# Kernel tuning notes

Hardware: AMD Instinct MI355X
Metric: run time of the kernel (lower is better)

Reference implementation:

```python
import jax, jax.numpy as jnp
import numpy as np

WIDTH = 16
HID = 512
NHEADS = 8
DK = HID // NHEADS
NLAYERS = 2
NHIGHWAY = 2
B = 4
S = 1024
PAD = S + 2 * WIDTH  # padded sequence length


def setup_inputs() -> dict:
    key = jax.random.key(0)
    ks = jax.random.split(key, 10)
    sc = 0.02
    f32 = jnp.float32
    return {
        "inputs": jax.random.normal(ks[0], (B, S, HID), f32),
        "masks": jnp.ones((B, S), jnp.int32),
        # 4 linears (q,k,v,out) per attention, torch Linear layout [out,in]
        "fw_lin_w": sc * jax.random.normal(ks[1], (NLAYERS, 4, HID, HID), f32),
        "fw_lin_b": jnp.zeros((NLAYERS, 4, HID), f32),
        "bw_lin_w": sc * jax.random.normal(ks[2], (NLAYERS, 4, HID, HID), f32),
        "bw_lin_b": jnp.zeros((NLAYERS, 4, HID), f32),
        # Highway: Linear(H, 2H); [:H]=nonlinear part, [H:]=gate (gate bias init 1)
        "fw_hw_w": sc * jax.random.normal(ks[3], (NLAYERS, NHIGHWAY, 2 * HID, HID), f32),
        "fw_hw_b": jnp.zeros((NLAYERS, NHIGHWAY, 2 * HID), f32).at[:, :, HID:].set(1.0),
        "bw_hw_w": sc * jax.random.normal(ks[4], (NLAYERS, NHIGHWAY, 2 * HID, HID), f32),
        "bw_hw_b": jnp.zeros((NLAYERS, NHIGHWAY, 2 * HID), f32).at[:, :, HID:].set(1.0),
        # learned boundary paddings, [width, hidden] per layer
        "fw_pad": sc * jax.random.normal(ks[5], (NLAYERS, WIDTH, HID), f32),
        "bw_pad": sc * jax.random.normal(ks[6], (NLAYERS, WIDTH, HID), f32),
        # relative-position weight vectors, [width+1] per layer
        "fw_rel": sc * jax.random.normal(ks[7], (NLAYERS, WIDTH + 1), f32),
        "bw_rel": sc * jax.random.normal(ks[8], (NLAYERS, WIDTH + 1), f32),
    }


def _band_masks():
    i = jnp.arange(PAD)[:, None]
    j = jnp.arange(PAD)[None, :]
    mf = (j <= i) & (j >= i - WIDTH - 1)          # causal band, width+2 wide
    mb = (j >= i) & (j <= i + WIDTH + 1)          # flipped (anticausal) band
    return mf, mb


def _mha(x, w, b, mask):
    # x: [B, PAD, HID]; w: [4, HID, HID]; b: [4, HID]
    def heads(t):
        return t.reshape(B, PAD, NHEADS, DK).transpose(0, 2, 1, 3)  # bhpd
    q = heads(x @ w[0].T + b[0])
    k = heads(x @ w[1].T + b[1])
    v = heads(x @ w[2].T + b[2])
    scores = jnp.einsum('bhqd,bhkd->bhqk', q, k) / np.sqrt(DK).astype(np.float32)
    scores = jnp.where(mask[None, None], scores, jnp.float32(-1e9))
    p = jax.nn.softmax(scores, axis=-1)
    o = jnp.einsum('bhqk,bhkd->bhqd', p, v)
    o = o.transpose(0, 2, 1, 3).reshape(B, PAD, HID)
    return o @ w[3].T + b[3]


def _highway(x, w, b):
    for i in range(NHIGHWAY):
        proj = x @ w[i].T + b[i]
        nonlin = jax.nn.relu(proj[..., :HID])
        gate = jax.nn.sigmoid(proj[..., HID:])
        x = gate * x + (1.0 - gate) * nonlin
    return x


def _rel(x, w, offset):
    # sum_k w[k] * x[:, offset+k : offset+k+S, :]  (width+1=17 fixed taps)
    out = w[0] * jax.lax.dynamic_slice_in_dim(x, offset, S, 1)
    for k in range(1, WIDTH + 1):
        out = out + w[k] * jax.lax.dynamic_slice_in_dim(x, offset + k, S, 1)
    return out


def _forward(inputs, fw_lin_w, fw_lin_b, bw_lin_w, bw_lin_b,
             fw_hw_w, fw_hw_b, bw_hw_w, bw_hw_b,
             fw_pad, bw_pad, fw_rel, bw_rel):
    mf, mb = _band_masks()
    f = inputs
    bk = inputs
    outs = []
    for l in range(NLAYERS):
        fp = jnp.broadcast_to(fw_pad[l][None], (B, WIDTH, HID))
        bp = jnp.broadcast_to(bw_pad[l][None], (B, WIDTH, HID))
        f_padded = jnp.concatenate([fp, f, bp], axis=1)    # [B, PAD, HID]
        b_padded = jnp.concatenate([fp, bk, bp], axis=1)
        fa = _mha(f_padded, fw_lin_w[l], fw_lin_b[l], mf)
        ba = _mha(b_padded, bw_lin_w[l], bw_lin_b[l], mb)
        # per-step: out[t] = attn[t+width] + rel-position windowed combination
        fo = fa[:, WIDTH:WIDTH + S, :] + _rel(fa, fw_rel[l], 0)
        bo = ba[:, WIDTH:WIDTH + S, :] + _rel(ba, bw_rel[l], WIDTH)
        f = _highway(fo, fw_hw_w[l], fw_hw_b[l])
        bk = _highway(bo, bw_hw_w[l], bw_hw_b[l])
        outs.append(jnp.concatenate([f, bk], axis=-1))
    return jnp.stack(outs, axis=0)  # [NLAYERS, B, S, 2*HID]


def reference(inputs, masks, fw_lin_w, fw_lin_b, bw_lin_w, bw_lin_b,
              fw_hw_w, fw_hw_b, bw_hw_w, bw_hw_b,
              fw_pad, bw_pad, fw_rel, bw_rel):
    # masks is accepted (as in the torch signature) but unused in the body
    return _forward(inputs, fw_lin_w, fw_lin_b, bw_lin_w, bw_lin_b,
                    fw_hw_w, fw_hw_b, bw_hw_w, bw_hw_b,
                    fw_pad, bw_pad, fw_rel, bw_rel)
```

## Files before the change

### kernel.cpp

```cpp
#include <hip/hip_runtime.h>

using s8 = __attribute__((ext_vector_type(8))) short;
using f4 = __attribute__((ext_vector_type(4))) float;

constexpr int WIDTH   = 16;
constexpr int HID     = 512;
constexpr int NHEADS  = 8;
constexpr int DK      = 64;
constexpr int NLAYERS = 2;
constexpr int NHW     = 2;
constexpr int B       = 4;
constexpr int S       = 1024;
constexpr int PAD     = S + 2 * WIDTH;
constexpr int RS      = 1024;
constexpr int K2      = 1024;

__device__ inline size_t caddr(int row, int col) {
    return ((size_t)((row >> 4) * 32 + (col >> 5)) << 9)
         + ((row & 15) << 3) + (((col >> 3) & 3) << 7) + (col & 7);
}

__device__ inline unsigned short f2bf(float x) {
    union { float f; unsigned u; } c; c.f = x;
    unsigned r = c.u + 0x7fffu + ((c.u >> 16) & 1u);
    return (unsigned short)(r >> 16);
}
__device__ inline float bf2f(unsigned short h) {
    union { float f; unsigned u; } c; c.u = ((unsigned)h) << 16; return c.f;
}
__device__ inline void split2(float x, unsigned short& h, unsigned short& l) {
    h = f2bf(x);
    l = f2bf(x - bf2f(h));
}
__device__ inline void store_split8(unsigned short* base, int row, int col,
                                    float4 v0, float4 v1) {
    float v[8] = {v0.x, v0.y, v0.z, v0.w, v1.x, v1.y, v1.z, v1.w};
    unsigned h[4], l[4];
    #pragma unroll
    for (int j = 0; j < 4; ++j) {
        unsigned short h0, l0, h1, l1;
        split2(v[2 * j], h0, l0); split2(v[2 * j + 1], h1, l1);
        h[j] = h0 | ((unsigned)h1 << 16);
        l[j] = l0 | ((unsigned)l1 << 16);
    }
    *(uint4*)(base + caddr(row, col))       = make_uint4(h[0], h[1], h[2], h[3]);
    *(uint4*)(base + caddr(row, col + 512)) = make_uint4(l[0], l[1], l[2], l[3]);
}
__device__ inline void store_split4_c(unsigned short* base, int row, int col,
                                      float4 v) {
    unsigned short h[4], l[4];
    split2(v.x, h[0], l[0]); split2(v.y, h[1], l[1]);
    split2(v.z, h[2], l[2]); split2(v.w, h[3], l[3]);
    uint2 hp, lp;
    hp.x = h[0] | ((unsigned)h[1] << 16); hp.y = h[2] | ((unsigned)h[3] << 16);
    lp.x = l[0] | ((unsigned)l[1] << 16); lp.y = l[2] | ((unsigned)l[3] << 16);
    *(uint2*)(base + caddr(row, col))       = hp;
    *(uint2*)(base + caddr(row, col + 512)) = lp;
}

__device__ inline void xcd_swizzle(int& bx, int& by) {
    const int gx = gridDim.x, gy = gridDim.y;
    const int nwg = gx * gy;
    const int orig = by * gx + bx;
    const int q = nwg >> 3, r = nwg & 7;
    const int x8 = orig & 7, i8 = orig >> 3;
    const int wg = (x8 < r ? x8 * (q + 1) : r * (q + 1) + (x8 - r) * q) + i8;
    bx = wg % gx;
    by = wg / gx;
}

__global__ __launch_bounds__(256) void build_pad_split(
    const float* __restrict__ src0, const float* __restrict__ src1,
    const float* __restrict__ front, const float* __restrict__ back,
    unsigned short* __restrict__ d0, unsigned short* __restrict__ d1)
{
    const float* x = blockIdx.z ? src1 : src0;
    unsigned short* xp2 = blockIdx.z ? d1 : d0;
    int idx = blockIdx.x * 256 + threadIdx.x;
    int c8 = idx & 63;
    int rest = idx >> 6;
    int p = rest % PAD;
    int b = rest / PAD;
    const float* s;
    if (p < WIDTH) {
        s = front + (size_t)p * HID;
    } else if (p < WIDTH + S) {
        s = x + ((size_t)b * S + (p - WIDTH)) * HID;
    } else {
        s = back + (size_t)(p - WIDTH - S) * HID;
    }
    float4 v0 = *(const float4*)(s + c8 * 8);
    float4 v1 = *(const float4*)(s + c8 * 8 + 4);
    store_split8(xp2, b * PAD + p, c8 * 8, v0, v1);
}

__global__ __launch_bounds__(256) void conv_w(
    const float* __restrict__ s0, const float* __restrict__ s1,
    unsigned short* __restrict__ w0, unsigned short* __restrict__ w1)
{
    const float* src = blockIdx.z ? s1 : s0;
    unsigned short* dst = blockIdx.z ? w1 : w0;
    int idx = blockIdx.x * 256 + threadIdx.x;
    int c8 = idx & 63;
    int r  = idx >> 6;
    float4 v0 = *(const float4*)(src + (size_t)r * HID + c8 * 8);
    float4 v1 = *(const float4*)(src + (size_t)r * HID + c8 * 8 + 4);
    store_split8(dst, r, c8 * 8, v0, v1);
}

__global__ __launch_bounds__(256) void conv_all(
    const float* __restrict__ fw_lin_w, const float* __restrict__ bw_lin_w,
    const float* __restrict__ fw_hw_w,  const float* __restrict__ bw_hw_w,
    unsigned short* __restrict__ w2all)
{
    int idx = blockIdx.x * 256 + threadIdx.x;
    int c8 = idx & 63;
    int r  = idx >> 6;
    int l  = r >> 12;
    int rr = r & 4095;
    const float* lin = blockIdx.z ? bw_lin_w : fw_lin_w;
    const float* hw  = blockIdx.z ? bw_hw_w  : fw_hw_w;
    const float* src;
    int drow;
    if (rr < 2048) {
        src  = lin + ((size_t)l * 2048 + rr) * HID;
        drow = blockIdx.z * 8192 + l * 4096 + rr;
    } else {
        int sub  = rr - 2048;
        int i_hw = sub >> 10;
        int rr2  = sub & 1023;
        int c    = rr2 & 511;
        int is_g = rr2 >> 9;
        int p    = ((c >> 4) << 5) + (c & 15) + (is_g << 4);
        src  = hw + ((size_t)l * 2048 + sub) * HID;
        drow = blockIdx.z * 8192 + l * 4096 + 2048 + (i_hw << 10) + p;
    }
    float4 v0 = *(const float4*)(src + c8 * 8);
    float4 v1 = *(const float4*)(src + c8 * 8 + 4);
    store_split8(w2all, drow, c8 * 8, v0, v1);
}

#define GLDS(src, dst) __builtin_amdgcn_global_load_lds(                        \
    (const __attribute__((address_space(1))) void*)(src),                       \
    (__attribute__((address_space(3))) void*)(dst), 16, 0, 0)

#define GEMM_CORE                                                               \
    __shared__ unsigned short Als[3][8 * 512];                                  \
    __shared__ unsigned short Bls[3][8 * 512];                                  \
    const int tid  = threadIdx.x;                                               \
    const int wave = tid >> 6;                                                  \
    const int lane = tid & 63;                                                  \
    int bx = blockIdx.x, by = blockIdx.y;                                       \
    xcd_swizzle(bx, by);                                                        \
    const int bm = by * 128;                                                    \
    const int bn = bx * 128;                                                    \
    const int wm = (wave >> 1) * 64;                                            \
    const int wn = (wave & 1) * 64;                                             \
    const unsigned short* SA0 = A  + ((size_t)((bm >> 4) + 2 * wave)     << 14) \
                                   + lane * 8;                                  \
    const unsigned short* SA1 = A  + ((size_t)((bm >> 4) + 2 * wave + 1) << 14) \
                                   + lane * 8;                                  \
    const unsigned short* SB0 = Bw + ((size_t)((bn >> 4) + 2 * wave)     << 14) \
                                   + lane * 8;                                  \
    const unsigned short* SB1 = Bw + ((size_t)((bn >> 4) + 2 * wave + 1) << 14) \
                                   + lane * 8;                                  \
    f4 acc[4][4] = {};                                                          \
    auto stage = [&](int slot, int kt) {                                        \
        const int ao = kt << 9;                                                 \
        const int bo = (kt & 15) << 9;                                          \
        GLDS(SA0 + ao, &Als[slot][(2 * wave)     * 512]);                       \
        GLDS(SA1 + ao, &Als[slot][(2 * wave + 1) * 512]);                       \
        GLDS(SB0 + bo, &Bls[slot][(2 * wave)     * 512]);                       \
        GLDS(SB1 + bo, &Bls[slot][(2 * wave + 1) * 512]);                       \
    };                                                                          \
    auto compute = [&](int slot) {                                              \
        s8 a[4], b[4];                                                          \
        _Pragma("unroll")                                                       \
        for (int i = 0; i < 4; ++i)                                             \
            a[i] = *(const s8*)&Als[slot][((wave >> 1) * 4 + i) * 512 + lane * 8];\
        _Pragma("unroll")                                                       \
        for (int j = 0; j < 4; ++j)                                             \
            b[j] = *(const s8*)&Bls[slot][((wave & 1) * 4 + j) * 512 + lane * 8];\
        __builtin_amdgcn_s_setprio(1);                                          \
        _Pragma("unroll")                                                       \
        for (int i = 0; i < 4; ++i)                                             \
            _Pragma("unroll")                                                   \
            for (int j = 0; j < 4; ++j)                                         \
                acc[i][j] = __builtin_amdgcn_mfma_f32_16x16x32_bf16(            \
                    a[i], b[j], acc[i][j], 0, 0, 0);                            \
        __builtin_amdgcn_s_setprio(0);                                          \
    };                                                                          \
    stage(0, 0);                                                                \
    stage(1, 1);                                                                \
    int rs_ = 0, ss_ = 2;                                                       \
    _Pragma("unroll 1")                                                         \
    for (int t = 0; t < 30; ++t) {                                              \
        asm volatile("s_waitcnt vmcnt(4)" ::: "memory");                        \
        __builtin_amdgcn_s_barrier();                                           \
        stage(ss_, t + 2);                                                      \
        compute(rs_);                                                           \
        rs_ = (rs_ == 2) ? 0 : rs_ + 1;                                         \
        ss_ = (ss_ == 2) ? 0 : ss_ + 1;                                         \
    }                                                                           \
    asm volatile("s_waitcnt vmcnt(4)" ::: "memory");                            \
    __builtin_amdgcn_s_barrier();                                               \
    compute(0);                                                    \
    asm volatile("s_waitcnt vmcnt(0)" ::: "memory");                            \
    __builtin_amdgcn_s_barrier();                                               \
    compute(1);

__global__ __launch_bounds__(256) void gemm_split(
    const unsigned short* __restrict__ A0, const unsigned short* __restrict__ B0,
    const float* __restrict__ bias0, float* __restrict__ C0,
    const unsigned short* __restrict__ A1, const unsigned short* __restrict__ B1,
    const float* __restrict__ bias1, float* __restrict__ C1,
    int N)
{
    const unsigned short* A  = blockIdx.z ? A1 : A0;
    const unsigned short* Bw = blockIdx.z ? B1 : B0;
    const float* bias        = blockIdx.z ? bias1 : bias0;
    float* C                 = blockIdx.z ? C1 : C0;

    GEMM_CORE

    const int col = lane & 15;
    const int rb  = (lane >> 4) * 4;
    #pragma unroll
    for (int j = 0; j < 4; ++j) {
        float bj = bias[bn + wn + j * 16 + col];
        #pragma unroll
        for (int i = 0; i < 4; ++i) {
            size_t base = (size_t)(bm + wm + i * 16 + rb) * N + (bn + wn + j * 16 + col);
            #pragma unroll
            for (int r = 0; r < 4; ++r)
                C[base + (size_t)r * N] = acc[i][j][r] + bj;
        }
    }
}

__global__ __launch_bounds__(256) void gemm_hw_fused(
    const unsigned short* __restrict__ A0, const unsigned short* __restrict__ B0,
    const float* __restrict__ hwb0, unsigned short* __restrict__ o2_0,
    float* __restrict__ dst0, float* __restrict__ osl0,
    const unsigned short* __restrict__ A1, const unsigned short* __restrict__ B1,
    const float* __restrict__ hwb1, unsigned short* __restrict__ o2_1,
    float* __restrict__ dst1, float* __restrict__ osl1,
    int first)
{
    const unsigned short* A  = blockIdx.z ? A1 : A0;
    const unsigned short* Bw = blockIdx.z ? B1 : B0;
    const float* hwb         = blockIdx.z ? hwb1 : hwb0;
    unsigned short* o2       = blockIdx.z ? o2_1 : o2_0;
    float* dstf              = blockIdx.z ? dst1 : dst0;
    float* osl               = blockIdx.z ? osl1 : osl0;

    GEMM_CORE

    const int col = lane & 15;
    const int rb  = (lane >> 4) * 4;
    #pragma unroll
    for (int jp = 0; jp < 2; ++jp) {
        const int cc = ((bn + wn) >> 1) + jp * 16 + col;
        const float bnl = hwb[cc];
        const float bg  = hwb[512 + cc];
        #pragma unroll
        for (int i = 0; i < 4; ++i) {
            #pragma unroll
            for (int r = 0; r < 4; ++r) {
                const int row = bm + wm + i * 16 + rb + r;
                float nl = acc[i][2 * jp][r] + bnl;
                float g  = acc[i][2 * jp + 1][r] + bg;
                float xv = bf2f(A[caddr(row, cc)])
                         + bf2f(A[caddr(row, cc + 512)]);
                float sg = 1.f / (1.f + __expf(-g));
                float o  = sg * xv + (1.f - sg) * fmaxf(nl, 0.f);
                if (first) {
                    unsigned short hh, ll; split2(o, hh, ll);
                    o2[caddr(row, cc)]       = hh;
                    o2[caddr(row, cc + 512)] = ll;
                } else {
                    dstf[(size_t)row * HID + cc]      = o;
                    osl[(size_t)row * (2 * HID) + cc] = o;
                }
            }
        }
    }
}

__global__ __launch_bounds__(256) void banded_attn(
    const float* __restrict__ Q0, const float* __restrict__ Q1,
    unsigned short* __restrict__ O0, unsigned short* __restrict__ O1,
    int dir0)
{
    const float* QKV = blockIdx.z ? Q1 : Q0;
    unsigned short* O2 = blockIdx.z ? O1 : O0;
    int backward = dir0 + blockIdx.z;

    int w    = blockIdx.x * 4 + (threadIdx.x >> 6);
    int lane = threadIdx.x & 63;
    int i  = w % PAD;
    int bh = w / PAD;
    int h  = bh & (NHEADS - 1);
    int b  = bh / NHEADS;

    int jlo, n;
    if (backward) { jlo = i; n = min(WIDTH + 2, PAD - i); }
    else          { jlo = max(0, i - WIDTH - 1); n = i - jlo + 1; }

    const int s = lane >> 4;
    const int d = lane & 15;
    const size_t rowbase = (size_t)(b * PAD) * 1536;
    const int colq = h * DK;

    float4 q4 = *(const float4*)(QKV + rowbase + (size_t)i * 1536 + colq + 4 * d);

    float sc[5];
    #pragma unroll
    for (int m = 0; m < 5; ++m) {
        int t  = 4 * m + s;
        int tc = t < n ? t : n - 1;
        float4 kv = *(const float4*)(QKV + rowbase + (size_t)(jlo + tc) * 1536
                                     + 512 + colq + 4 * d);
        float p = q4.x * kv.x + q4.y * kv.y + q4.z * kv.z + q4.w * kv.w;
        p += __shfl_xor(p, 1);
        p += __shfl_xor(p, 2);
        p += __shfl_xor(p, 4);
        p += __shfl_xor(p, 8);
        sc[m] = p * 0.125f;
    }

    float sv[WIDTH + 2];
    #pragma unroll
    for (int t = 0; t < WIDTH + 2; ++t) {
        float v = __shfl(sc[t >> 2], (t & 3) << 4);
        sv[t] = (t < n) ? v : -1e30f;
    }
    float mx = sv[0];
    #pragma unroll
    for (int t = 1; t < WIDTH + 2; ++t) mx = fmaxf(mx, sv[t]);
    float denom = 0.f;
    #pragma unroll
    for (int t = 0; t < WIDTH + 2; ++t) { sv[t] = __expf(sv[t] - mx); denom += sv[t]; }
    float inv = 1.0f / denom;

    float od0 = 0.f, od1 = 0.f;
    #pragma unroll
    for (int t = 0; t < WIDTH + 2; t += 2) {
        int tc0 = t     < n ? t     : n - 1;
        int tc1 = t + 1 < n ? t + 1 : n - 1;
        od0 += sv[t]     * QKV[rowbase + (size_t)(jlo + tc0) * 1536 + 1024 + colq + lane];
        od1 += sv[t + 1] * QKV[rowbase + (size_t)(jlo + tc1) * 1536 + 1024 + colq + lane];
    }
    float od = (od0 + od1) * inv;

    unsigned short hh, ll;
    split2(od, hh, ll);
    const int orow = b * PAD + i;
    O2[caddr(orow, colq + lane)]       = hh;
    O2[caddr(orow, colq + lane + 512)] = ll;
}

__global__ __launch_bounds__(256) void rel_combine(
    const float* __restrict__ a0, const float* __restrict__ a1,
    const float* __restrict__ w0, const float* __restrict__ w1,
    unsigned short* __restrict__ f0, unsigned short* __restrict__ f1,
    int off0, int off1)
{
    const float* att = blockIdx.z ? a1 : a0;
    const float* w   = blockIdx.z ? w1 : w0;
    unsigned short* fo2 = blockIdx.z ? f1 : f0;
    int offset = blockIdx.z ? off1 : off0;

    int idx = blockIdx.x * 256 + threadIdx.x;
    int c8 = idx & 63;
    int rest = idx >> 6;
    int t = rest & (S - 1);
    int b = rest >> 10;

    const float* rowbase = att + (size_t)b * PAD * HID + c8 * 8;
    float4 acc0 = *(const float4*)(rowbase + (size_t)(WIDTH + t) * HID);
    float4 acc1 = *(const float4*)(rowbase + (size_t)(WIDTH + t) * HID + 4);
    #pragma unroll
    for (int k = 0; k <= WIDTH; ++k) {
        float wk = w[k];
        float4 x0 = *(const float4*)(rowbase + (size_t)(offset + k + t) * HID);
        float4 x1 = *(const float4*)(rowbase + (size_t)(offset + k + t) * HID + 4);
        acc0.x += wk * x0.x; acc0.y += wk * x0.y;
        acc0.z += wk * x0.z; acc0.w += wk * x0.w;
        acc1.x += wk * x1.x; acc1.y += wk * x1.y;
        acc1.z += wk * x1.z; acc1.w += wk * x1.w;
    }
    store_split8(fo2, b * S + t, c8 * 8, acc0, acc1);
}

__global__ __launch_bounds__(256) void highway_gate(
    const unsigned short* __restrict__ x0, const unsigned short* __restrict__ x1,
    const float* __restrict__ p0, const float* __restrict__ p1,
    float* __restrict__ of0, float* __restrict__ of1,
    unsigned short* __restrict__ o20, unsigned short* __restrict__ o21,
    float* __restrict__ os0, float* __restrict__ os1)
{
    const unsigned short* x2 = blockIdx.z ? x1 : x0;
    const float* proj        = blockIdx.z ? p1 : p0;
    float* outf              = blockIdx.z ? of1 : of0;
    unsigned short* out2     = blockIdx.z ? o21 : o20;
    float* oslice            = blockIdx.z ? os1 : os0;

    int idx = blockIdx.x * 256 + threadIdx.x;
    int c4 = idx & 127;
    int r  = idx >> 7;
    uint2 hp = *(const uint2*)(x2 + caddr(r, c4 * 4));
    uint2 lp = *(const uint2*)(x2 + caddr(r, c4 * 4 + 512));
    float4 xv;
    xv.x = bf2f((unsigned short)(hp.x & 0xffff)) + bf2f((unsigned short)(lp.x & 0xffff));
    xv.y = bf2f((unsigned short)(hp.x >> 16))    + bf2f((unsigned short)(lp.x >> 16));
    xv.z = bf2f((unsigned short)(hp.y & 0xffff)) + bf2f((unsigned short)(lp.y & 0xffff));
    xv.w = bf2f((unsigned short)(hp.y >> 16))    + bf2f((unsigned short)(lp.y >> 16));

    float4 nl = *(const float4*)(proj + (size_t)r * (2 * HID) + c4 * 4);
    float4 g  = *(const float4*)(proj + (size_t)r * (2 * HID) + HID + c4 * 4);
    float4 o;
    float sg;
    sg = 1.f / (1.f + __expf(-g.x)); o.x = sg * xv.x + (1.f - sg) * fmaxf(nl.x, 0.f);
    sg = 1.f / (1.f + __expf(-g.y)); o.y = sg * xv.y + (1.f - sg) * fmaxf(nl.y, 0.f);
    sg = 1.f / (1.f + __expf(-g.z)); o.z = sg * xv.z + (1.f - sg) * fmaxf(nl.z, 0.f);
    sg = 1.f / (1.f + __expf(-g.w)); o.w = sg * xv.w + (1.f - sg) * fmaxf(nl.w, 0.f);
    if (outf)   *(float4*)(outf + (size_t)idx * 4) = o;
    if (out2)   store_split4_c(out2, r, c4 * 4, o);
    if (oslice) *(float4*)(oslice + (size_t)r * (2 * HID) + c4 * 4) = o;
}

extern "C" void kernel_launch(void* const* d_in, const int* in_sizes, int n_in,
                              void* d_out, int out_size, void* d_ws, size_t ws_size,
                              hipStream_t stream)
{
    const float* inputs   = (const float*)d_in[0];
    const float* fw_lin_w = (const float*)d_in[2];
    const float* fw_lin_b = (const float*)d_in[3];
    const float* bw_lin_w = (const float*)d_in[4];
    const float* bw_lin_b = (const float*)d_in[5];
    const float* fw_hw_w  = (const float*)d_in[6];
    const float* fw_hw_b  = (const float*)d_in[7];
    const float* bw_hw_w  = (const float*)d_in[8];
    const float* bw_hw_b  = (const float*)d_in[9];
    const float* fw_pad   = (const float*)d_in[10];
    const float* bw_pad   = (const float*)d_in[11];
    const float* fw_rel   = (const float*)d_in[12];
    const float* bw_rel   = (const float*)d_in[13];
    float* out = (float*)d_out;
    float* ws  = (float*)d_ws;

    const size_t BSH  = (size_t)B * S * HID;
    const size_t QKVF = (size_t)B * PAD * 1536;
    const int MP = B * PAD;
    const int MS = B * S;

    const size_t GROUPED_FLOATS = 2 * QKVF + (2 * (size_t)MP * RS + 2 * (size_t)1536 * RS) / 2;
    const size_t WALL_FLOATS    = 2 * QKVF + (2 * (size_t)MP * RS + (size_t)2 * 8192 * RS) / 2;
    const bool wall    = ws_size >= WALL_FLOATS * 4;
    const bool grouped = wall || ws_size >= GROUPED_FLOATS * 4;
    const int G = grouped ? 2 : 1;

    float* f  = ws;
    float* bk = f + BSH;

    float* QKV[2]; float* ATT[2]; float* HWP[2];
    unsigned short* ACT2[2]; unsigned short* W2[2];
    unsigned short* ACT2B[2] = {nullptr, nullptr};
    unsigned short* w2all = nullptr;
    if (grouped) {
        QKV[0] = ws;             QKV[1] = ws + QKVF;
        float* extra = ws + 2 * BSH;
        ATT[0] = extra;          ATT[1] = extra + (size_t)MP * HID;
        HWP[0] = extra;          HWP[1] = extra + (size_t)MS * 1024;
        ACT2B[0] = (unsigned short*)extra;
        ACT2B[1] = ACT2B[0] + (size_t)MS * RS;
        unsigned short* a2 = (unsigned short*)(ws + 2 * QKVF);
        ACT2[0] = a2;            ACT2[1] = a2 + (size_t)MP * RS;
        unsigned short* w2 = a2 + 2 * (size_t)MP * RS;
        if (wall) { w2all = w2; W2[0] = W2[1] = nullptr; }
        else      { W2[0] = w2; W2[1] = w2 + (size_t)1536 * RS; }
    } else {
        float* qkvS = bk + BSH;
        QKV[0] = QKV[1] = qkvS;
        ATT[0] = ATT[1] = qkvS;
        HWP[0] = HWP[1] = qkvS;
        unsigned short* a2 = (unsigned short*)(qkvS + QKVF);
        ACT2[0] = ACT2[1] = a2;
        W2[0] = W2[1] = a2 + (size_t)MP * RS;
    }

    if (wall) {
        conv_all<<<dim3(8192 * 64 / 256, 1, 2), 256, 0, stream>>>(
            fw_lin_w, bw_lin_w, fw_hw_w, bw_hw_w, w2all);
    }
    auto WB = [&](int dir, int l, int seg) -> unsigned short* {
        return w2all + ((size_t)dir * 8192 + (size_t)l * 4096 + seg) * RS;
    };

    for (int l = 0; l < NLAYERS; ++l) {
        const float* LINW[2] = {fw_lin_w + (size_t)l * 4 * HID * HID,
                                bw_lin_w + (size_t)l * 4 * HID * HID};
        const float* LINB[2] = {fw_lin_b + (size_t)l * 4 * HID,
                                bw_lin_b + (size_t)l * 4 * HID};
        const float* HWW[2]  = {fw_hw_w + (size_t)l * NHW * 2 * HID * HID,
                                bw_hw_w + (size_t)l * NHW * 2 * HID * HID};
        const float* HWB[2]  = {fw_hw_b + (size_t)l * NHW * 2 * HID,
                                bw_hw_b + (size_t)l * NHW * 2 * HID};
        const float* RELW[2] = {fw_rel + (size_t)l * (WIDTH + 1),
                                bw_rel + (size_t)l * (WIDTH + 1)};
        const float* front = fw_pad + (size_t)l * WIDTH * HID;
        const float* back  = bw_pad + (size_t)l * WIDTH * HID;
        float* DST[2] = {f, bk};
        float* OSL[2] = {out + (size_t)l * B * S * 2 * HID,
                         out + (size_t)l * B * S * 2 * HID + HID};
        const float* SRC[2] = {(l == 0) ? inputs : f, (l == 0) ? inputs : bk};

        for (int d0 = 0; d0 < 2; d0 += G) {
            const int dB = (G == 2) ? 1 : d0;

            build_pad_split<<<dim3(MP * 64 / 256, 1, G), 256, 0, stream>>>(
                SRC[d0], SRC[dB], front, back, ACT2[0], ACT2[1]);

            unsigned short *wq0, *wq1;
            if (wall) { wq0 = WB(d0, l, 0); wq1 = WB(dB, l, 0); }
            else {
                conv_w<<<dim3(1536 * 64 / 256, 1, G), 256, 0, stream>>>(
                    LINW[d0], LINW[dB], W2[0], W2[1]);
                wq0 = W2[0]; wq1 = W2[1];
            }
            gemm_split<<<dim3(1536 / 128, MP / 128, G), 256, 0, stream>>>(
                ACT2[0], wq0, LINB[d0], QKV[0],
                ACT2[1], wq1, LINB[dB], QKV[1], 1536);

            banded_attn<<<dim3(B * NHEADS * PAD / 4, 1, G), 256, 0, stream>>>(
                QKV[0], QKV[1], ACT2[0], ACT2[1], d0);

            unsigned short *wo0, *wo1;
            if (wall) { wo0 = WB(d0, l, 1536); wo1 = WB(dB, l, 1536); }
            else {
                conv_w<<<dim3(512 * 64 / 256, 1, G), 256, 0, stream>>>(
                    LINW[d0] + 3 * (size_t)HID * HID, LINW[dB] + 3 * (size_t)HID * HID,
                    W2[0], W2[1]);
                wo0 = W2[0]; wo1 = W2[1];
            }
            gemm_split<<<dim3(512 / 128, MP / 128, G), 256, 0, stream>>>(
                ACT2[0], wo0, LINB[d0] + 3 * HID, ATT[0],
                ACT2[1], wo1, LINB[dB] + 3 * HID, ATT[1], 512);

            rel_combine<<<dim3(MS * 64 / 256, 1, G), 256, 0, stream>>>(
                ATT[0], ATT[1], RELW[d0], RELW[dB], ACT2[0], ACT2[1],
                d0 * WIDTH, dB * WIDTH);

            if (wall) {
                gemm_hw_fused<<<dim3(1024 / 128, MS / 128, G), 256, 0, stream>>>(
                    ACT2[0], WB(d0, l, 2048), HWB[d0], ACT2B[0], nullptr, nullptr,
                    ACT2[1], WB(dB, l, 2048), HWB[dB], ACT2B[1], nullptr, nullptr, 1);
                gemm_hw_fused<<<dim3(1024 / 128, MS / 128, G), 256, 0, stream>>>(
                    ACT2B[0], WB(d0, l, 3072), HWB[d0] + 1024, nullptr, DST[d0], OSL[d0],
                    ACT2B[1], WB(dB, l, 3072), HWB[dB] + 1024, nullptr, DST[dB], OSL[dB], 0);
            } else {
                for (int i = 0; i < NHW; ++i) {
                    conv_w<<<dim3(1024 * 64 / 256, 1, G), 256, 0, stream>>>(
                        HWW[d0] + (size_t)i * 2 * HID * HID,
                        HWW[dB] + (size_t)i * 2 * HID * HID, W2[0], W2[1]);
                    gemm_split<<<dim3(1024 / 128, MS / 128, G), 256, 0, stream>>>(
                        ACT2[0], W2[0], HWB[d0] + (size_t)i * 2 * HID, HWP[0],
                        ACT2[1], W2[1], HWB[dB] + (size_t)i * 2 * HID, HWP[1], 1024);
                    const bool last = (i == NHW - 1);
                    highway_gate<<<dim3(MS * 128 / 256, 1, G), 256, 0, stream>>>(
                        ACT2[0], ACT2[1], HWP[0], HWP[1],
                        last ? DST[d0] : (float*)nullptr,
                        last ? DST[dB] : (float*)nullptr,
                        last ? (unsigned short*)nullptr : ACT2[0],
                        last ? (unsigned short*)nullptr : ACT2[1],
                        last ? OSL[d0] : (float*)nullptr,
                        last ? OSL[dB] : (float*)nullptr);
                }
            }
        }
    }
}
```

Measured before the change: 577.9 us.

## Load GEMM B fragments directly into registers instead of staging through LDS

The GEMM core no longer stages the B (weight) tiles through shared memory. Each wave now loads its own B fragments from global memory straight into a three-deep register ring, while A still uses global_load_lds triple buffering. The main loop is fully unrolled, waitcnt thresholds are adjusted, and launch bounds request three blocks per CU. This halves LDS traffic and footprint per block, but B tiles are now loaded redundantly by the two waves sharing a column and register pressure rises.

```diff
diff --git a/kernel.cpp b/kernel.cpp
--- a/kernel.cpp
+++ b/kernel.cpp
@@ -146,7 +146,6 @@
 
 #define GEMM_CORE                                                               \
     __shared__ unsigned short Als[3][8 * 512];                                  \
-    __shared__ unsigned short Bls[3][8 * 512];                                  \
     const int tid  = threadIdx.x;                                               \
     const int wave = tid >> 6;                                                  \
     const int lane = tid & 63;                                                  \
@@ -160,56 +159,50 @@
                                    + lane * 8;                                  \
     const unsigned short* SA1 = A  + ((size_t)((bm >> 4) + 2 * wave + 1) << 14) \
                                    + lane * 8;                                  \
-    const unsigned short* SB0 = Bw + ((size_t)((bn >> 4) + 2 * wave)     << 14) \
-                                   + lane * 8;                                  \
-    const unsigned short* SB1 = Bw + ((size_t)((bn >> 4) + 2 * wave + 1) << 14) \
-                                   + lane * 8;                                  \
+    const unsigned short* pb[4];                                                \
+    _Pragma("unroll")                                                           \
+    for (int j = 0; j < 4; ++j)                                                 \
+        pb[j] = Bw + ((size_t)((((bn + wn) >> 4) + j) * 32) << 9) + lane * 8;   \
     f4 acc[4][4] = {};                                                          \
-    auto stage = [&](int slot, int kt) {                                        \
+    s8 bfr[3][4];                                                               \
+    auto stageA = [&](int slot, int kt) {                                       \
         const int ao = kt << 9;                                                 \
-        const int bo = (kt & 15) << 9;                                          \
         GLDS(SA0 + ao, &Als[slot][(2 * wave)     * 512]);                       \
         GLDS(SA1 + ao, &Als[slot][(2 * wave + 1) * 512]);                       \
-        GLDS(SB0 + bo, &Bls[slot][(2 * wave)     * 512]);                       \
-        GLDS(SB1 + bo, &Bls[slot][(2 * wave + 1) * 512]);                       \
     };                                                                          \
-    auto compute = [&](int slot) {                                              \
-        s8 a[4], b[4];                                                          \
+    stageA(0, 0);                                                               \
+    _Pragma("unroll")                                                           \
+    for (int j = 0; j < 4; ++j) bfr[0][j] = *(const s8*)(pb[j]);                \
+    stageA(1, 1);                                                               \
+    _Pragma("unroll")                                                           \
+    for (int j = 0; j < 4; ++j) bfr[1][j] = *(const s8*)(pb[j] + 512);          \
+    _Pragma("unroll")                                                           \
+    for (int t = 0; t < 32; ++t) {                                              \
+        if (t == 31) asm volatile("s_waitcnt vmcnt(0)" ::: "memory");           \
+        else         asm volatile("s_waitcnt vmcnt(6)" ::: "memory");           \
+        __builtin_amdgcn_s_barrier();                                           \
+        if (t < 30) {                                                           \
+            stageA((t + 2) % 3, t + 2);                                         \
+            const int bo = ((t + 2) & 15) << 9;                                 \
+            _Pragma("unroll")                                                   \
+            for (int j = 0; j < 4; ++j)                                         \
+                bfr[(t + 2) % 3][j] = *(const s8*)(pb[j] + bo);                 \
+        }                                                                       \
+        s8 a[4];                                                                \
         _Pragma("unroll")                                                       \
         for (int i = 0; i < 4; ++i)                                             \
-            a[i] = *(const s8*)&Als[slot][((wave >> 1) * 4 + i) * 512 + lane * 8];\
-        _Pragma("unroll")                                                       \
-        for (int j = 0; j < 4; ++j)                                             \
-            b[j] = *(const s8*)&Bls[slot][((wave & 1) * 4 + j) * 512 + lane * 8];\
+            a[i] = *(const s8*)&Als[t % 3][((wave >> 1) * 4 + i) * 512 + lane * 8];\
         __builtin_amdgcn_s_setprio(1);                                          \
         _Pragma("unroll")                                                       \
         for (int i = 0; i < 4; ++i)                                             \
             _Pragma("unroll")                                                   \
             for (int j = 0; j < 4; ++j)                                         \
                 acc[i][j] = __builtin_amdgcn_mfma_f32_16x16x32_bf16(            \
-                    a[i], b[j], acc[i][j], 0, 0, 0);                            \
+                    a[i], bfr[t % 3][j], acc[i][j], 0, 0, 0);                   \
         __builtin_amdgcn_s_setprio(0);                                          \
-    };                                                                          \
-    stage(0, 0);                                                                \
-    stage(1, 1);                                                                \
-    int rs_ = 0, ss_ = 2;                                                       \
-    _Pragma("unroll 1")                                                         \
-    for (int t = 0; t < 30; ++t) {                                              \
-        asm volatile("s_waitcnt vmcnt(4)" ::: "memory");                        \
-        __builtin_amdgcn_s_barrier();                                           \
-        stage(ss_, t + 2);                                                      \
-        compute(rs_);                                                           \
-        rs_ = (rs_ == 2) ? 0 : rs_ + 1;                                         \
-        ss_ = (ss_ == 2) ? 0 : ss_ + 1;                                         \
-    }                                                                           \
-    asm volatile("s_waitcnt vmcnt(4)" ::: "memory");                            \
-    __builtin_amdgcn_s_barrier();                                               \
-    compute(0);                                                    \
-    asm volatile("s_waitcnt vmcnt(0)" ::: "memory");                            \
-    __builtin_amdgcn_s_barrier();                                               \
-    compute(1);
-
-__global__ __launch_bounds__(256) void gemm_split(
+    }
+
+__global__ __launch_bounds__(256, 3) void gemm_split(
     const unsigned short* __restrict__ A0, const unsigned short* __restrict__ B0,
     const float* __restrict__ bias0, float* __restrict__ C0,
     const unsigned short* __restrict__ A1, const unsigned short* __restrict__ B1,
@@ -238,7 +231,7 @@
     }
 }
 
-__global__ __launch_bounds__(256) void gemm_hw_fused(
+__global__ __launch_bounds__(256, 3) void gemm_hw_fused(
     const unsigned short* __restrict__ A0, const unsigned short* __restrict__ B0,
     const float* __restrict__ hwb0, unsigned short* __restrict__ o2_0,
     float* __restrict__ dst0, float* __restrict__ osl0,
```

Result: faster. 519.7 us (-10.1%).
